# Kernel tuning notes

Measured on AMD Instinct MI355X. Metric: run time of the kernel, lower is better.

Reference implementation:

```python
import jax, jax.numpy as jnp
import numpy as np
import math

B, T, D, H = 2, 2048, 1024, 16
DH = D // H          # 64
NB = DH // 2         # 32 rotary pairs
EPS = 1e-5


def setup_inputs() -> dict:
    key = jax.random.key(0)
    ks = jax.random.split(key, 20)
    x = jax.random.normal(ks[0], (B, T, D), dtype=jnp.float32)
    angles = jax.random.uniform(ks[1], (B, H, T, NB), dtype=jnp.float32) * (2.0 * math.pi)
    cos_a = jnp.cos(angles)
    sin_a = jnp.sin(angles)
    sigma = jax.random.uniform(ks[2], (B, T, H, NB), dtype=jnp.float32)
    causal_mask = jnp.triu(jnp.ones((T, T), dtype=bool), k=1)  # True above diag -> masked
    w = lambda k, i, o: jax.random.normal(k, (i, o), dtype=jnp.float32) * 0.02
    return {
        "x": x, "cos_a": cos_a, "sin_a": sin_a, "sigma": sigma, "causal_mask": causal_mask,
        "ln1_g": jnp.ones((D,), jnp.float32), "ln1_b": jnp.zeros((D,), jnp.float32),
        "wq": w(ks[3], D, D), "bq": jnp.zeros((D,), jnp.float32),
        "wk": w(ks[4], D, D), "bk": jnp.zeros((D,), jnp.float32),
        "wv": w(ks[5], D, D), "bv": jnp.zeros((D,), jnp.float32),
        "wo": w(ks[6], D, D), "bo": jnp.zeros((D,), jnp.float32),
        "ln2_g": jnp.ones((D,), jnp.float32), "ln2_b": jnp.zeros((D,), jnp.float32),
        "w1": w(ks[7], D, 4 * D), "b1": jnp.zeros((4 * D,), jnp.float32),
        "w2": w(ks[8], 4 * D, D), "b2": jnp.zeros((D,), jnp.float32),
    }


def _layer_norm(x, g, b):
    mu = jnp.mean(x, axis=-1, keepdims=True)
    var = jnp.mean(jnp.square(x - mu), axis=-1, keepdims=True)
    return (x - mu) * jax.lax.rsqrt(var + EPS) * g + b


def _apply_rope(q, cos_a, sin_a):
    # q: (B,H,T,DH); rotate even/odd pairs by per-pair angles (B,H,T,NB)
    q1 = q[..., 0::2]
    q2 = q[..., 1::2]
    re = q1 * cos_a - q2 * sin_a
    im = q1 * sin_a + q2 * cos_a
    return jnp.stack([re, im], axis=-1).reshape(q.shape)


def reference(x, cos_a, sin_a, sigma, causal_mask,
              ln1_g, ln1_b, wq, bq, wk, bk, wv, bv, wo, bo,
              ln2_g, ln2_b, w1, b1, w2, b2):
    h = _layer_norm(x, ln1_g, ln1_b)
    Q = (h @ wq + bq).reshape(B, T, H, DH).transpose(0, 2, 1, 3)
    K = (h @ wk + bk).reshape(B, T, H, DH).transpose(0, 2, 1, 3)
    V = (h @ wv + bv).reshape(B, T, H, DH).transpose(0, 2, 1, 3)
    Q = _apply_rope(Q, cos_a, sin_a)
    K = _apply_rope(K, cos_a, sin_a)
    # per-(B,H,T) temperature from mean uncertainty
    temp = 1.0 + jnp.mean(sigma, axis=-1).transpose(0, 2, 1)  # (B,H,T)
    scale = math.sqrt(DH)
    scores = jnp.einsum("bhtd,bhsd->bhts", Q, K) / (scale * temp[..., None])
    scores = jnp.where(causal_mask[None, None], -jnp.inf, scores)
    attn = jax.nn.softmax(scores, axis=-1)
    out = jnp.einsum("bhts,bhsd->bhtd", attn, V)
    out = out.transpose(0, 2, 1, 3).reshape(B, T, D)
    x = x + (out @ wo + bo)
    h2 = _layer_norm(x, ln2_g, ln2_b)
    ffn = jax.nn.gelu(h2 @ w1 + b1, approximate=False) @ w2 + b2
    return x + ffn
```

## Files before the change

### kernel.cpp

```cpp
#include <hip/hip_runtime.h>

typedef unsigned short ushort;
typedef unsigned int uint;

typedef __attribute__((ext_vector_type(8))) short short8;
typedef __attribute__((ext_vector_type(8))) unsigned short ushort8;
typedef __attribute__((ext_vector_type(4))) unsigned short ushort4v;
typedef __attribute__((ext_vector_type(4))) float f32x4;
typedef __attribute__((ext_vector_type(4))) uint uint4v;

#define DEV static __device__ __forceinline__

DEV ushort f2b(float f){
  union { float f; uint u; } v; v.f = f;
  uint u = v.u;
  u += 0x7fffu + ((u >> 16) & 1u);
  return (ushort)(u >> 16);
}
DEV float b2f(ushort h){
  union { uint u; float f; } v; v.u = ((uint)h) << 16;
  return v.f;
}
DEV uint cvt_pk_bf16(float lo, float hi){
  uint r;
  asm("v_cvt_pk_bf16_f32 %0, %1, %2" : "=v"(r) : "v"(lo), "v"(hi));
  return r;
}
DEV ushort f2b1(float f){ return (ushort)cvt_pk_bf16(f, f); }
DEV float exp2v(float x){
  float r;
  asm("v_exp_f32 %0, %1" : "=v"(r) : "v"(x));
  return r;
}
DEV float gelu_f(float x){
  float z = fabsf(x) * 0.70710678118654752f;
  float t = __builtin_amdgcn_rcpf(1.f + 0.3275911f * z);
  float poly = t * (0.254829592f + t * (-0.284496736f + t * (1.421413741f +
               t * (-1.453152027f + t * 1.061405429f))));
  float e = exp2v(-z * z * 1.44269504088896f);
  float erf_abs = 1.f - poly * e;
  float erf_s = copysignf(erf_abs, x);
  return 0.5f * x * (1.f + erf_s);
}

constexpr int Bc = 2, Tc = 2048, Dc = 1024, Hc = 16, DHc = 64, NBc = 32;
constexpr int Rc = Bc * Tc;
constexpr int D4c = 4 * Dc;

__global__ __launch_bounds__(256) void k_transcvt_all(
    const float* __restrict__ wq, const float* __restrict__ wk, const float* __restrict__ wv,
    const float* __restrict__ wo, const float* __restrict__ w1, const float* __restrict__ w2,
    ushort* __restrict__ wqT, ushort* __restrict__ wkT, ushort* __restrict__ wvT,
    ushort* __restrict__ woT, ushort* __restrict__ w1T, ushort* __restrict__ w2T){
  __shared__ float tile[32][33];
  const int bid = blockIdx.x;
  const float* in; ushort* out; int K, N, bx, by;
  if (bid < 4096){
    int seg = bid >> 10, loc = bid & 1023;
    in  = seg == 0 ? wq  : seg == 1 ? wk  : seg == 2 ? wv  : wo;
    out = seg == 0 ? wqT : seg == 1 ? wkT : seg == 2 ? wvT : woT;
    K = 1024; N = 1024; bx = loc & 31; by = loc >> 5;
  } else if (bid < 8192){
    int loc = bid - 4096;
    in = w1; out = w1T; K = 1024; N = 4096; bx = loc & 127; by = loc >> 7;
  } else {
    int loc = bid - 8192;
    in = w2; out = w2T; K = 4096; N = 1024; bx = loc & 31; by = loc >> 5;
  }
  int n0 = bx * 32, k0 = by * 32;
  int c = threadIdx.x & 31, r0 = threadIdx.x >> 5;
#pragma unroll
  for (int i = 0; i < 4; i++){
    int k = r0 + i * 8;
    tile[k][c] = in[(size_t)(k0 + k) * N + n0 + c];
  }
  __syncthreads();
#pragma unroll
  for (int i = 0; i < 4; i++){
    int n = r0 + i * 8;
    out[(size_t)(n0 + n) * K + k0 + c] = f2b(tile[c][n]);
  }
}

__global__ __launch_bounds__(256) void k_ln(const float* __restrict__ x, const float* __restrict__ g,
                                            const float* __restrict__ bb, ushort* __restrict__ out){
  int row = blockIdx.x, tid = threadIdx.x;
  const f32x4* xr = (const f32x4*)(x + (size_t)row * Dc);
  f32x4 v = xr[tid];
  float s  = v.x + v.y + v.z + v.w;
  float ss = v.x*v.x + v.y*v.y + v.z*v.z + v.w*v.w;
#pragma unroll
  for (int off = 32; off > 0; off >>= 1){
    s  += __shfl_xor(s,  off, 64);
    ss += __shfl_xor(ss, off, 64);
  }
  __shared__ float red[2][4];
  int w = tid >> 6;
  if ((tid & 63) == 0){ red[0][w] = s; red[1][w] = ss; }
  __syncthreads();
  s  = red[0][0] + red[0][1] + red[0][2] + red[0][3];
  ss = red[1][0] + red[1][1] + red[1][2] + red[1][3];
  float mu  = s * (1.f / Dc);
  float var = ss * (1.f / Dc) - mu * mu;
  float rs  = rsqrtf(var + 1e-5f);
  f32x4 gv = ((const f32x4*)g)[tid];
  f32x4 bv = ((const f32x4*)bb)[tid];
  ushort4v o;
  o.x = f2b((v.x - mu) * rs * gv.x + bv.x);
  o.y = f2b((v.y - mu) * rs * gv.y + bv.y);
  o.z = f2b((v.z - mu) * rs * gv.z + bv.z);
  o.w = f2b((v.w - mu) * rs * gv.w + bv.w);
  ((ushort4v*)(out + (size_t)row * Dc))[tid] = o;
}

#define GLDS(src, dst) __builtin_amdgcn_global_load_lds( \
    (const __attribute__((address_space(1))) void*)(src), \
    (__attribute__((address_space(3))) void*)(dst), 16, 0, 0)

#define XCD_SWZ(bx_, by_, nbx_, nwg_) do{ \
  int lid_ = blockIdx.y * (nbx_) + blockIdx.x; \
  int cpx_ = (nwg_) >> 3; \
  int swz_ = (lid_ & 7) * cpx_ + (lid_ >> 3); \
  bx_ = swz_ % (nbx_); by_ = swz_ / (nbx_); \
}while(0)

#define STAGE128(nb_, k0_) do { \
  _Pragma("unroll") \
  for (int i_ = 0; i_ < 4; i_++){ \
    int chunk_ = w * 4 + i_; \
    GLDS(A  + (size_t)(m0 + chunk_ * 8 + rloc) * K + (k0_) + gsrc * 8, &SM[nb_][0][chunk_ * 512]); \
    GLDS(Bt + (size_t)(n0 + chunk_ * 8 + rloc) * K + (k0_) + gsrc * 8, &SM[nb_][1][chunk_ * 512]); \
  } \
} while(0)

#define GEMM_CORE(cb_) do { \
  _Pragma("unroll") \
  for (int ks = 0; ks < 2; ks++){ \
    const int gs = (ks * 4 + lg) ^ l7; \
    short8 aF[4], bF[4]; \
    _Pragma("unroll") \
    for (int mi = 0; mi < 4; mi++) aF[mi] = *(const short8*)&SM[cb_][0][(arow + mi * 16) * 64 + gs * 8]; \
    _Pragma("unroll") \
    for (int ni = 0; ni < 4; ni++) bF[ni] = *(const short8*)&SM[cb_][1][(brow + ni * 16) * 64 + gs * 8]; \
    _Pragma("unroll") \
    for (int mi = 0; mi < 4; mi++) \
      _Pragma("unroll") \
      for (int ni = 0; ni < 4; ni++) \
        acc[mi][ni] = __builtin_amdgcn_mfma_f32_16x16x32_bf16(aF[mi], bF[ni], acc[mi][ni], 0, 0, 0); \
  } \
} while(0)

template<int OUT_BF16, int ACT_GELU, int HAS_RES>
__global__ __launch_bounds__(256) void k_gemm(const ushort* __restrict__ A, const ushort* __restrict__ Bt,
                                              const float* __restrict__ bias, const float* __restrict__ resid,
                                              void* __restrict__ Cout, int M, int N, int K){
  __shared__ ushort SM[2][2][8192];
  const int tid = threadIdx.x;
  int bx, by;
  XCD_SWZ(bx, by, N >> 7, (M >> 7) * (N >> 7));
  const int m0 = by * 128, n0 = bx * 128;
  const int w = tid >> 6, lane = tid & 63;
  const int wr = w >> 1, wc = w & 1;
  const int la15 = lane & 15, lg = lane >> 4, l7 = lane & 7;
  const int rloc = lane >> 3, gsrc = (lane & 7) ^ rloc;

  f32x4 acc[4][4];
#pragma unroll
  for (int i = 0; i < 4; i++)
#pragma unroll
    for (int j = 0; j < 4; j++) acc[i][j] = f32x4{0.f, 0.f, 0.f, 0.f};

  const int arow = wr * 64 + la15;
  const int brow = wc * 64 + la15;

  STAGE128(0, 0);
  __syncthreads();
  const int NT = K >> 6;
  for (int t = 0; t < NT; t++){
    const int cb = t & 1;
    if (t + 1 < NT) STAGE128(cb ^ 1, (t + 1) << 6);
    GEMM_CORE(cb);
    __syncthreads();
  }

  if (OUT_BF16){
    ushort* Cs = &SM[0][0][0];
#pragma unroll
    for (int mi = 0; mi < 4; mi++)
#pragma unroll
      for (int ni = 0; ni < 4; ni++){
        int ccl = wc * 64 + ni * 16 + la15;
        float bv = bias[n0 + ccl];
        f32x4 a4 = acc[mi][ni];
#pragma unroll
        for (int r = 0; r < 4; r++){
          int rl = wr * 64 + mi * 16 + lg * 4 + r;
          float v = a4[r] + bv;
          if (ACT_GELU) v = gelu_f(v);
          Cs[rl * 136 + ccl] = f2b1(v);
        }
      }
    __syncthreads();
#pragma unroll
    for (int p = 0; p < 8; p++){
      int row = p * 16 + (tid >> 4);
      int col = (tid & 15) * 8;
      ushort8 vv = *(const ushort8*)&Cs[row * 136 + col];
      *(ushort8*)((ushort*)Cout + (size_t)(m0 + row) * N + n0 + col) = vv;
    }
  } else {
#pragma unroll
    for (int mi = 0; mi < 4; mi++)
#pragma unroll
      for (int ni = 0; ni < 4; ni++){
        int cc = n0 + wc * 64 + ni * 16 + la15;
        float bv = bias[cc];
        f32x4 a4 = acc[mi][ni];
#pragma unroll
        for (int r = 0; r < 4; r++){
          int rr = m0 + wr * 64 + mi * 16 + lg * 4 + r;
          float v = a4[r] + bv;
          if (HAS_RES) v += resid[(size_t)rr * N + cc];
          ((float*)Cout)[(size_t)rr * N + cc] = v;
        }
      }
  }
}

__global__ __launch_bounds__(256) void k_gemm_n64(const ushort* __restrict__ A, const ushort* __restrict__ Bt,
                                                  const float* __restrict__ bias, const float* __restrict__ resid,
                                                  float* __restrict__ Cout, int M, int N, int K){
  __shared__ ushort SM[2][12288];
  const int tid = threadIdx.x;
  int bx, by;
  XCD_SWZ(bx, by, N >> 6, (M >> 7) * (N >> 6));
  const int m0 = by * 128, n0 = bx * 64;
  const int w = tid >> 6, lane = tid & 63;
  const int la15 = lane & 15, lg = lane >> 4, l7 = lane & 7;
  const int rloc = lane >> 3, gsrc = (lane & 7) ^ rloc;

  f32x4 acc[2][4];
#pragma unroll
  for (int i = 0; i < 2; i++)
#pragma unroll
    for (int j = 0; j < 4; j++) acc[i][j] = f32x4{0.f, 0.f, 0.f, 0.f};

  const int arow = w * 32 + la15;

#define STAGE64(nb_, k0_) do { \
  _Pragma("unroll") \
  for (int i_ = 0; i_ < 4; i_++){ \
    int chunk_ = w * 4 + i_; \
    GLDS(A + (size_t)(m0 + chunk_ * 8 + rloc) * K + (k0_) + gsrc * 8, &SM[nb_][chunk_ * 512]); \
  } \
  _Pragma("unroll") \
  for (int j_ = 0; j_ < 2; j_++){ \
    int chunk_ = w * 2 + j_; \
    GLDS(Bt + (size_t)(n0 + chunk_ * 8 + rloc) * K + (k0_) + gsrc * 8, &SM[nb_][8192 + chunk_ * 512]); \
  } \
} while(0)

#define CORE64(cb_) do { \
  _Pragma("unroll") \
  for (int ks = 0; ks < 2; ks++){ \
    const int gs = (ks * 4 + lg) ^ l7; \
    short8 aF[2], bF[4]; \
    _Pragma("unroll") \
    for (int mi = 0; mi < 2; mi++) aF[mi] = *(const short8*)&SM[cb_][(arow + mi * 16) * 64 + gs * 8]; \
    _Pragma("unroll") \
    for (int ni = 0; ni < 4; ni++) bF[ni] = *(const short8*)&SM[cb_][8192 + (ni * 16 + la15) * 64 + gs * 8]; \
    _Pragma("unroll") \
    for (int mi = 0; mi < 2; mi++) \
      _Pragma("unroll") \
      for (int ni = 0; ni < 4; ni++) \
        acc[mi][ni] = __builtin_amdgcn_mfma_f32_16x16x32_bf16(aF[mi], bF[ni], acc[mi][ni], 0, 0, 0); \
  } \
} while(0)

  STAGE64(0, 0);
  __syncthreads();
  const int NT = K >> 6;
  for (int t = 0; t < NT; t++){
    const int cb = t & 1;
    if (t + 1 < NT) STAGE64(cb ^ 1, (t + 1) << 6);
    CORE64(cb);
    __syncthreads();
  }

#pragma unroll
  for (int mi = 0; mi < 2; mi++)
#pragma unroll
    for (int ni = 0; ni < 4; ni++){
      int cc = n0 + ni * 16 + la15;
      float bv = bias[cc];
      f32x4 a4 = acc[mi][ni];
#pragma unroll
      for (int r = 0; r < 4; r++){
        int rr = m0 + w * 32 + mi * 16 + lg * 4 + r;
        float v = a4[r] + bv + resid[(size_t)rr * N + cc];
        Cout[(size_t)rr * N + cc] = v;
      }
    }
}

__global__ __launch_bounds__(256) void k_gemm_qkv(const ushort* __restrict__ A, const ushort* __restrict__ Bt,
                                                  const float* __restrict__ bq_, const float* __restrict__ bk_,
                                                  const float* __restrict__ bv_, ushort* __restrict__ oq,
                                                  ushort* __restrict__ ok, ushort* __restrict__ ovt,
                                                  const float* __restrict__ cosa, const float* __restrict__ sina,
                                                  int K){
  __shared__ ushort SM[2][2][8192];
  const int tid = threadIdx.x;
  int bx, by;
  XCD_SWZ(bx, by, 24, 24 * 32);
  const int m0 = by * 128, n0 = bx * 128;
  const int w = tid >> 6, lane = tid & 63;
  const int wr = w >> 1, wc = w & 1;
  const int la15 = lane & 15, lg = lane >> 4, l7 = lane & 7;
  const int rloc = lane >> 3, gsrc = (lane & 7) ^ rloc;

  f32x4 acc[4][4];
#pragma unroll
  for (int i = 0; i < 4; i++)
#pragma unroll
    for (int j = 0; j < 4; j++) acc[i][j] = f32x4{0.f, 0.f, 0.f, 0.f};

  const int arow = wr * 64 + la15;
  const int brow = wc * 64 + la15;

  STAGE128(0, 0);
  __syncthreads();
  const int NT = K >> 6;
  for (int t = 0; t < NT; t++){
    const int cb = t & 1;
    if (t + 1 < NT) STAGE128(cb ^ 1, (t + 1) << 6);
    GEMM_CORE(cb);
    __syncthreads();
  }
  __syncthreads();

  const int sel = n0 >> 10;
  ushort* Cs = &SM[0][0][0];
  if (sel < 2){
    const float* bias = sel == 0 ? bq_ : bk_;
    ushort* o = sel == 0 ? oq : ok;
#pragma unroll
    for (int mi = 0; mi < 4; mi++)
#pragma unroll
      for (int ni = 0; ni < 4; ni++){
        int ccl = wc * 64 + ni * 16 + la15;
        float bv = bias[(n0 & 1023) + ccl];
        f32x4 a4 = acc[mi][ni];
#pragma unroll
        for (int r = 0; r < 4; r++){
          int rl = wr * 64 + mi * 16 + lg * 4 + r;
          Cs[rl * 136 + ccl] = f2b1(a4[r] + bv);
        }
      }
    __syncthreads();
#pragma unroll
    for (int p = 0; p < 8; p++){
      int row = p * 16 + (tid >> 4);
      int col = (tid & 15) * 8;
      ushort8 vv = *(const ushort8*)&Cs[row * 136 + col];
      int rr = m0 + row;
      int bb2 = rr >> 11, tt2 = rr & 2047;
      int cg = (n0 & 1023) + col;
      int hh2 = cg >> 6;
      int nb0 = (cg & 63) >> 1;
      size_t ai = ((size_t)(bb2 * Hc + hh2) * Tc + tt2) * NBc + nb0;
      f32x4 cv = *(const f32x4*)(cosa + ai);
      f32x4 sv = *(const f32x4*)(sina + ai);
      ushort8 ov;
#pragma unroll
      for (int j2 = 0; j2 < 4; j2++){
        float x1 = b2f((ushort)vv[2 * j2]), x2 = b2f((ushort)vv[2 * j2 + 1]);
        uint pk = cvt_pk_bf16(x1 * cv[j2] - x2 * sv[j2], x1 * sv[j2] + x2 * cv[j2]);
        ov[2 * j2]     = (ushort)(pk & 0xffff);
        ov[2 * j2 + 1] = (ushort)(pk >> 16);
      }
      *(ushort8*)(o + (size_t)rr * Dc + cg) = ov;
    }
  } else {
#pragma unroll
    for (int mi = 0; mi < 4; mi++)
#pragma unroll
      for (int ni = 0; ni < 4; ni++){
        int ccl = wc * 64 + ni * 16 + la15;
        float bv = bv_[(n0 - 2048) + ccl];
        f32x4 a4 = acc[mi][ni];
#pragma unroll
        for (int r = 0; r < 4; r++){
          int rl = wr * 64 + mi * 16 + lg * 4 + r;
          Cs[ccl * 136 + rl] = f2b1(a4[r] + bv);
        }
      }
    __syncthreads();
    const int bb = m0 >> 11, t0 = m0 & 2047;
#pragma unroll
    for (int p = 0; p < 8; p++){
      int nl = p * 16 + (tid >> 4);
      int tl = (tid & 15) * 8;
      ushort8 vv = *(const ushort8*)&Cs[nl * 136 + tl];
      int ng = (n0 - 2048) + nl;
      *(ushort8*)(ovt + ((size_t)(bb * 1024 + ng) << 11) + t0 + tl) = vv;
    }
  }
}

__global__ __launch_bounds__(256) void k_iscale(const float* __restrict__ sigma, float* __restrict__ isc){
  int idx = blockIdx.x * 256 + threadIdx.x;
  int hh = idx & 15;
  int t  = (idx >> 4) & 2047;
  int b  = idx >> 15;
  const f32x4* sp = (const f32x4*)(sigma + (size_t)idx * NBc);
  float s = 0.f;
#pragma unroll
  for (int i = 0; i < 8; i++){ f32x4 v = sp[i]; s += v.x + v.y + v.z + v.w; }
  isc[(b * Hc + hh) * Tc + t] = 1.44269504088896f / (8.f * (1.f + s * (1.f / NBc)));
}

__global__ __launch_bounds__(64) void k_attn_mfma(const ushort* __restrict__ qb, const ushort* __restrict__ kb,
                                                  const ushort* __restrict__ vtb, const float* __restrict__ isc,
                                                  ushort* __restrict__ ao){
  __shared__ ushort smem[8192];
  const int bid = blockIdx.x;
  const int bh = bid & 31, b = bh >> 4, h = bh & 15;
  const int qt = 63 - (bid >> 5);
  const int lane = threadIdx.x;
  const int la15 = lane & 15, lg = lane >> 4, l7 = lane & 7;
  const int q0w = qt * 32;

  short8 qf[2][2];
  float iscv[2];
#pragma unroll
  for (int sub = 0; sub < 2; sub++){
    int qg = q0w + sub * 16 + la15;
    size_t rb = (size_t)(b * Tc + qg) * Dc + h * DHc;
    qf[sub][0] = *(const short8*)(qb + rb + lg * 8);
    qf[sub][1] = *(const short8*)(qb + rb + 32 + lg * 8);
    iscv[sub] = isc[bh * Tc + qg];
  }

  f32x4 O[2][4];
#pragma unroll
  for (int sub = 0; sub < 2; sub++)
#pragma unroll
    for (int dt = 0; dt < 4; dt++) O[sub][dt] = f32x4{0.f, 0.f, 0.f, 0.f};
  float lacc[2] = {0.f, 0.f};

  const ushort* kbase  = kb + (size_t)b * Tc * Dc + h * DHc;
  const ushort* vtbase = vtb + (size_t)bh * DHc * Tc;
  const int ktmax = q0w + 31;

  const int Rl = lane >> 3, sl = lane & 7;
  const int gV = sl ^ (Rl & 7);

#define STAGE_KV(kt_) do { \
  _Pragma("unroll") \
  for (int i_ = 0; i_ < 8; i_++){ \
    int R_ = i_ * 8 + Rl; \
    int gk_ = sl ^ ((R_ & 3) ^ (((R_ >> 3) & 3) << 1)); \
    GLDS(kbase + (size_t)((kt_) + R_) * Dc + gk_ * 8, &smem[i_ * 512]); \
    GLDS(vtbase + (size_t)R_ * Tc + (kt_) + gV * 8, &smem[4096 + i_ * 512]); \
  } \
} while(0)

#define COMPUTE_T(kt_) do { \
  _Pragma("unroll") \
  for (int sub = 0; sub < 2; sub++){ \
    f32x4 s_[4]; \
    __builtin_amdgcn_s_setprio(1); \
    _Pragma("unroll") \
    for (int t_ = 0; t_ < 4; t_++){ \
      s_[t_] = f32x4{0.f, 0.f, 0.f, 0.f}; \
      s_[t_] = __builtin_amdgcn_mfma_f32_16x16x32_bf16(kf[t_][0], qf[sub][0], s_[t_], 0, 0, 0); \
      s_[t_] = __builtin_amdgcn_mfma_f32_16x16x32_bf16(kf[t_][1], qf[sub][1], s_[t_], 0, 0, 0); \
    } \
    __builtin_amdgcn_s_setprio(0); \
    const int qg_ = q0w + sub * 16 + la15; \
    const float sc_ = iscv[sub]; \
    const bool diag_ = ((kt_) + 63 > q0w + sub * 16); \
    uint up_[4][2]; \
    float lp_ = 0.f; \
    _Pragma("unroll") \
    for (int t_ = 0; t_ < 4; t_++){ \
      _Pragma("unroll") \
      for (int pr_ = 0; pr_ < 2; pr_++){ \
        float e0_ = exp2v(s_[t_][2 * pr_] * sc_); \
        float e1_ = exp2v(s_[t_][2 * pr_ + 1] * sc_); \
        if (diag_){ \
          int kp0_ = (kt_) + ((t_ >> 1) << 5) + lg * 8 + ((t_ & 1) << 2) + 2 * pr_; \
          if (kp0_ > qg_)     e0_ = 0.f; \
          if (kp0_ + 1 > qg_) e1_ = 0.f; \
        } \
        lp_ += e0_ + e1_; \
        up_[t_][pr_] = cvt_pk_bf16(e0_, e1_); \
      } \
    } \
    lacc[sub] += lp_; \
    __builtin_amdgcn_s_setprio(1); \
    _Pragma("unroll") \
    for (int kh_ = 0; kh_ < 2; kh_++){ \
      union { uint4v w; short8 s8; } pfr_; \
      pfr_.w[0] = up_[kh_ * 2][0];     pfr_.w[1] = up_[kh_ * 2][1]; \
      pfr_.w[2] = up_[kh_ * 2 + 1][0]; pfr_.w[3] = up_[kh_ * 2 + 1][1]; \
      _Pragma("unroll") \
      for (int dt_ = 0; dt_ < 4; dt_++) \
        O[sub][dt_] = __builtin_amdgcn_mfma_f32_16x16x32_bf16(vtf[dt_][kh_], pfr_.s8, O[sub][dt_], 0, 0, 0); \
    } \
    __builtin_amdgcn_s_setprio(0); \
  } \
} while(0)

  STAGE_KV(0);
  asm volatile("s_waitcnt vmcnt(0)" ::: "memory");
  __builtin_amdgcn_sched_barrier(0);

  for (int kt = 0;; kt += 64){
    short8 kf[4][2], vtf[4][2];
#pragma unroll
    for (int t_ = 0; t_ < 4; t_++){
      int r = ((t_ >> 1) << 5) + ((la15 >> 2) << 3) + ((t_ & 1) << 2) + (la15 & 3);
#pragma unroll
      for (int ds = 0; ds < 2; ds++){
        int g = (ds * 4 + lg) ^ ((la15 & 3) ^ ((la15 >> 2) << 1));
        kf[t_][ds] = *(const short8*)&smem[r * 64 + g * 8];
      }
    }
#pragma unroll
    for (int dt = 0; dt < 4; dt++){
      int d = dt * 16 + la15;
#pragma unroll
      for (int kh = 0; kh < 2; kh++){
        int g = (kh * 4 + lg) ^ (la15 & 7);
        vtf[dt][kh] = *(const short8*)&smem[4096 + d * 64 + g * 8];
      }
    }
    asm volatile("s_waitcnt lgkmcnt(0)" ::: "memory");
    __builtin_amdgcn_sched_barrier(0);
    STAGE_KV(kt + 64);
    COMPUTE_T(kt);
    if (kt + 64 > ktmax) break;
    asm volatile("s_waitcnt vmcnt(0)" ::: "memory");
    __builtin_amdgcn_sched_barrier(0);
  }
  asm volatile("s_waitcnt vmcnt(0)" ::: "memory");
  __builtin_amdgcn_sched_barrier(0);

  char* osb = (char*)smem;
#pragma unroll
  for (int sub = 0; sub < 2; sub++){
    float lt = lacc[sub];
    lt += __shfl_xor(lt, 16, 64);
    lt += __shfl_xor(lt, 32, 64);
    float inv = 1.f / lt;
#pragma unroll
    for (int dt = 0; dt < 4; dt++)
#pragma unroll
      for (int pr = 0; pr < 2; pr++){
        uint u = cvt_pk_bf16(O[sub][dt][2 * pr] * inv, O[sub][dt][2 * pr + 1] * inv);
        *(uint*)(osb + (sub * 16 + la15) * 136 + (dt * 16 + lg * 4 + pr * 2) * 2) = u;
      }
  }
#pragma unroll
  for (int it = 0; it < 4; it++){
    int ql = it * 8 + (lane >> 3);
    ushort8 v = *(const ushort8*)(osb + ql * 136 + l7 * 16);
    *(ushort8*)(ao + (size_t)(b * Tc + q0w + ql) * Dc + h * DHc + l7 * 8) = v;
  }
}

extern "C" void kernel_launch(void* const* d_in, const int* in_sizes, int n_in,
                              void* d_out, int out_size, void* d_ws, size_t ws_size,
                              hipStream_t stream){
  (void)in_sizes; (void)n_in; (void)out_size; (void)ws_size;
  const float* x    = (const float*)d_in[0];
  const float* cosa = (const float*)d_in[1];
  const float* sina = (const float*)d_in[2];
  const float* sigma= (const float*)d_in[3];
  const float* ln1g = (const float*)d_in[5];
  const float* ln1b = (const float*)d_in[6];
  const float* wq   = (const float*)d_in[7];
  const float* bq   = (const float*)d_in[8];
  const float* wk   = (const float*)d_in[9];
  const float* bk   = (const float*)d_in[10];
  const float* wv   = (const float*)d_in[11];
  const float* bv   = (const float*)d_in[12];
  const float* wo   = (const float*)d_in[13];
  const float* bo   = (const float*)d_in[14];
  const float* ln2g = (const float*)d_in[15];
  const float* ln2b = (const float*)d_in[16];
  const float* w1   = (const float*)d_in[17];
  const float* b1   = (const float*)d_in[18];
  const float* w2   = (const float*)d_in[19];
  const float* b2   = (const float*)d_in[20];
  float* out = (float*)d_out;

  char* ws = (char*)d_ws;
  constexpr size_t MB = 1024 * 1024;
  ushort* wqT  = (ushort*)(ws +  0 * MB);
  ushort* wkT  = (ushort*)(ws +  2 * MB);
  ushort* wvT  = (ushort*)(ws +  4 * MB);
  ushort* woT  = (ushort*)(ws +  6 * MB);
  ushort* w1T  = (ushort*)(ws +  8 * MB);
  ushort* w2T  = (ushort*)(ws + 16 * MB);
  ushort* hb   = (ushort*)(ws + 24 * MB);
  ushort* qbuf = (ushort*)(ws + 32 * MB);
  ushort* kbuf = (ushort*)(ws + 40 * MB);
  ushort* vtb  = (ushort*)(ws + 48 * MB);
  ushort* aob  = (ushort*)(ws + 56 * MB);
  float*  x2   = (float*)(ws + 64 * MB);
  float*  iscp = (float*)(ws + 80 * MB);
  ushort* g1b  = qbuf;

  k_transcvt_all<<<12288, 256, 0, stream>>>(wq, wk, wv, wo, w1, w2, wqT, wkT, wvT, woT, w1T, w2T);
  k_ln<<<Rc, 256, 0, stream>>>(x, ln1g, ln1b, hb);
  k_gemm_qkv<<<dim3(3 * Dc / 128, Rc / 128), 256, 0, stream>>>(hb, wqT, bq, bk, bv, qbuf, kbuf, vtb,
                                                               cosa, sina, Dc);
  k_iscale<<<(Bc * Tc * Hc) / 256, 256, 0, stream>>>(sigma, iscp);
  k_attn_mfma<<<dim3(2048), 64, 0, stream>>>(qbuf, kbuf, vtb, iscp, aob);
  k_gemm_n64<<<dim3(Dc / 64, Rc / 128), 256, 0, stream>>>(aob, woT, bo, x, x2, Rc, Dc, Dc);
  k_ln<<<Rc, 256, 0, stream>>>(x2, ln2g, ln2b, hb);
  k_gemm<1, 1, 0><<<dim3(D4c / 128, Rc / 128), 256, 0, stream>>>(hb, w1T, b1, nullptr, g1b, Rc, D4c, Dc);
  k_gemm_n64<<<dim3(Dc / 64, Rc / 128), 256, 0, stream>>>(g1b, w2T, b2, x2, out, Rc, Dc, D4c);
}
```

Before: 227.8 us.

## Double-buffer attention K/V staging and drop XCD block swizzle in GEMMs

```diff
diff --git a/kernel.cpp b/kernel.cpp
--- a/kernel.cpp
+++ b/kernel.cpp
@@ -117,13 +117,6 @@
     (const __attribute__((address_space(1))) void*)(src), \
     (__attribute__((address_space(3))) void*)(dst), 16, 0, 0)
 
-#define XCD_SWZ(bx_, by_, nbx_, nwg_) do{ \
-  int lid_ = blockIdx.y * (nbx_) + blockIdx.x; \
-  int cpx_ = (nwg_) >> 3; \
-  int swz_ = (lid_ & 7) * cpx_ + (lid_ >> 3); \
-  bx_ = swz_ % (nbx_); by_ = swz_ / (nbx_); \
-}while(0)
-
 #define STAGE128(nb_, k0_) do { \
   _Pragma("unroll") \
   for (int i_ = 0; i_ < 4; i_++){ \
@@ -156,9 +149,7 @@
                                               void* __restrict__ Cout, int M, int N, int K){
   __shared__ ushort SM[2][2][8192];
   const int tid = threadIdx.x;
-  int bx, by;
-  XCD_SWZ(bx, by, N >> 7, (M >> 7) * (N >> 7));
-  const int m0 = by * 128, n0 = bx * 128;
+  const int m0 = blockIdx.y * 128, n0 = blockIdx.x * 128;
   const int w = tid >> 6, lane = tid & 63;
   const int wr = w >> 1, wc = w & 1;
   const int la15 = lane & 15, lg = lane >> 4, l7 = lane & 7;
@@ -232,9 +223,7 @@
                                                   float* __restrict__ Cout, int M, int N, int K){
   __shared__ ushort SM[2][12288];
   const int tid = threadIdx.x;
-  int bx, by;
-  XCD_SWZ(bx, by, N >> 6, (M >> 7) * (N >> 6));
-  const int m0 = by * 128, n0 = bx * 64;
+  const int m0 = blockIdx.y * 128, n0 = blockIdx.x * 64;
   const int w = tid >> 6, lane = tid & 63;
   const int la15 = lane & 15, lg = lane >> 4, l7 = lane & 7;
   const int rloc = lane >> 3, gsrc = (lane & 7) ^ rloc;
@@ -311,9 +300,7 @@
                                                   int K){
   __shared__ ushort SM[2][2][8192];
   const int tid = threadIdx.x;
-  int bx, by;
-  XCD_SWZ(bx, by, 24, 24 * 32);
-  const int m0 = by * 128, n0 = bx * 128;
+  const int m0 = blockIdx.y * 128, n0 = blockIdx.x * 128;
   const int w = tid >> 6, lane = tid & 63;
   const int wr = w >> 1, wc = w & 1;
   const int la15 = lane & 15, lg = lane >> 4, l7 = lane & 7;
@@ -423,7 +410,7 @@
 __global__ __launch_bounds__(64) void k_attn_mfma(const ushort* __restrict__ qb, const ushort* __restrict__ kb,
                                                   const ushort* __restrict__ vtb, const float* __restrict__ isc,
                                                   ushort* __restrict__ ao){
-  __shared__ ushort smem[8192];
+  __shared__ ushort smem[16384];
   const int bid = blockIdx.x;
   const int bh = bid & 31, b = bh >> 4, h = bh & 15;
   const int qt = 63 - (bid >> 5);
@@ -456,13 +443,13 @@
   const int Rl = lane >> 3, sl = lane & 7;
   const int gV = sl ^ (Rl & 7);
 
-#define STAGE_KV(kt_) do { \
+#define STAGE_KV(kt_, c_) do { \
   _Pragma("unroll") \
   for (int i_ = 0; i_ < 8; i_++){ \
     int R_ = i_ * 8 + Rl; \
     int gk_ = sl ^ ((R_ & 3) ^ (((R_ >> 3) & 3) << 1)); \
-    GLDS(kbase + (size_t)((kt_) + R_) * Dc + gk_ * 8, &smem[i_ * 512]); \
-    GLDS(vtbase + (size_t)R_ * Tc + (kt_) + gV * 8, &smem[4096 + i_ * 512]); \
+    GLDS(kbase + (size_t)((kt_) + R_) * Dc + gk_ * 8, &smem[(c_) * 4096 + i_ * 512]); \
+    GLDS(vtbase + (size_t)R_ * Tc + (kt_) + gV * 8, &smem[8192 + (c_) * 4096 + i_ * 512]); \
   } \
 } while(0)
 
@@ -513,19 +500,22 @@
   } \
 } while(0)
 
-  STAGE_KV(0);
+  STAGE_KV(0, 0);
   asm volatile("s_waitcnt vmcnt(0)" ::: "memory");
   __builtin_amdgcn_sched_barrier(0);
 
+  int cur = 0;
   for (int kt = 0;; kt += 64){
+    STAGE_KV(kt + 64, cur ^ 1);
     short8 kf[4][2], vtf[4][2];
+    const int kofs = cur * 4096, vofs = 8192 + cur * 4096;
 #pragma unroll
     for (int t_ = 0; t_ < 4; t_++){
       int r = ((t_ >> 1) << 5) + ((la15 >> 2) << 3) + ((t_ & 1) << 2) + (la15 & 3);
 #pragma unroll
       for (int ds = 0; ds < 2; ds++){
         int g = (ds * 4 + lg) ^ ((la15 & 3) ^ ((la15 >> 2) << 1));
-        kf[t_][ds] = *(const short8*)&smem[r * 64 + g * 8];
+        kf[t_][ds] = *(const short8*)&smem[kofs + r * 64 + g * 8];
       }
     }
 #pragma unroll
@@ -534,16 +524,14 @@
 #pragma unroll
       for (int kh = 0; kh < 2; kh++){
         int g = (kh * 4 + lg) ^ (la15 & 7);
-        vtf[dt][kh] = *(const short8*)&smem[4096 + d * 64 + g * 8];
+        vtf[dt][kh] = *(const short8*)&smem[vofs + d * 64 + g * 8];
       }
     }
-    asm volatile("s_waitcnt lgkmcnt(0)" ::: "memory");
-    __builtin_amdgcn_sched_barrier(0);
-    STAGE_KV(kt + 64);
     COMPUTE_T(kt);
     if (kt + 64 > ktmax) break;
     asm volatile("s_waitcnt vmcnt(0)" ::: "memory");
     __builtin_amdgcn_sched_barrier(0);
+    cur ^= 1;
   }
   asm volatile("s_waitcnt vmcnt(0)" ::: "memory");
   __builtin_amdgcn_sched_barrier(0);
```

Result: no change. 231.0 us (+1.4%).
